# Kernel tuning notes

Measured on AMD Instinct MI355X. Metric: run time of the kernel, lower is better.

Reference implementation:

```python
import jax, jax.numpy as jnp
import numpy as np
from jax import lax

NUM_HEADS = 8  # init_kwargs: num_heads
TOPK = 7       # hard-coded in DMF.forward


def setup_inputs() -> dict:
    key = jax.random.key(0)
    k1, k2, k3, k4 = jax.random.split(key, 4)
    b, dim, H, W = 8, 384, 128, 128
    x = jax.random.normal(k1, (b, dim, H, W), dtype=jnp.float32)
    qkv_w = jax.random.normal(k2, (dim * 3, dim), dtype=jnp.float32) * 0.05   # 1x1 conv weight
    dw_w = jax.random.normal(k3, (dim * 3, 1, 3, 3), dtype=jnp.float32) * 0.05  # depthwise 3x3
    proj_w = jax.random.normal(k4, (dim, dim), dtype=jnp.float32) * 0.05     # 1x1 conv weight
    temperature = jnp.ones((NUM_HEADS, 1, 1), dtype=jnp.float32)
    return {"x": x, "qkv_w": qkv_w, "dw_w": dw_w, "proj_w": proj_w, "temperature": temperature}


def _l2norm(t, eps=1e-12):
    # matches torch.nn.functional.normalize(dim=-1)
    n = jnp.sqrt(jnp.sum(t * t, axis=-1, keepdims=True))
    return t / jnp.maximum(n, eps)


def reference(x, qkv_w, dw_w, proj_w, temperature):
    b, c, h, w = x.shape
    ch = c // NUM_HEADS  # channels per head

    # 1x1 conv (pointwise) -> depthwise 3x3 conv
    qkv = jnp.einsum('bchw,oc->bohw', x, qkv_w)
    qkv = lax.conv_general_dilated(
        qkv, dw_w, window_strides=(1, 1), padding=[(1, 1), (1, 1)],
        feature_group_count=qkv.shape[1],
        dimension_numbers=('NCHW', 'OIHW', 'NCHW'))
    q, k, v = jnp.split(qkv, 3, axis=1)

    def to_heads(t):  # b (head ch) h w -> b head ch (h w)
        return t.reshape(b, NUM_HEADS, ch, h * w)

    q = _l2norm(to_heads(q))
    k = _l2norm(to_heads(k))
    v = to_heads(v)

    # channel attention: [b, head, ch, ch]
    attn_weight = jnp.einsum('bhcn,bhdn->bhcd', q, k) * temperature

    # top-k sparsify along last dim, then masked softmax
    _, idx = lax.top_k(attn_weight, TOPK)                      # [b,h,ch,TOPK]
    cols = jnp.arange(attn_weight.shape[-1])
    mask = (idx[..., None] == cols).any(axis=-2)               # [b,h,ch,ch] bool
    attn = jnp.where(mask, attn_weight, -jnp.inf)
    attn = jax.nn.softmax(attn, axis=-1)

    out = jnp.einsum('bhcd,bhdn->bhcn', attn, v).reshape(b, c, h, w)
    out = jnp.einsum('bchw,oc->bohw', out, proj_w)
    return out
```

## Files before the change

kernel.cpp:

```cpp
#include <hip/hip_runtime.h>

#define HWN 16384
#define WDIM 128

typedef __bf16 bf16x8 __attribute__((ext_vector_type(8)));
typedef __bf16 bf16x4 __attribute__((ext_vector_type(4)));
typedef __bf16 bf16x2 __attribute__((ext_vector_type(2)));
typedef float floatx4 __attribute__((ext_vector_type(4)));

#define LSTR 36

__global__ __launch_bounds__(256, 2) void gemm_mfma3(
    const __bf16* __restrict__ Ah, const __bf16* __restrict__ Al,
    const float* __restrict__ B, float* __restrict__ C,
    int K, long sA, long sB, long sC) {
  __shared__ __bf16 sAh[128 * LSTR], sAl[128 * LSTR], sBh[128 * LSTR], sBl[128 * LSTR];
  const int bz = blockIdx.z;
  Ah += (long)bz * sA;
  Al += (long)bz * sA;
  B += (long)bz * sB;
  C += (long)bz * sC;
  const int tid = threadIdx.x;
  const int n0 = blockIdx.x << 7, m0 = blockIdx.y << 7;
  const int arow = tid >> 1, akq = (tid & 1) << 4;
  const int bn = (tid & 63) << 1;
  const int bkb = (tid >> 6) << 3;
  const int lane = tid & 63, wv = tid >> 6;
  const int mq = (wv & 1) << 6, nq = (wv >> 1) << 6;
  const int fm = lane & 15, fq = lane >> 4;
  floatx4 acc[4][4] = {};
  for (int k0 = 0; k0 < K; k0 += 32) {
    const __bf16* pAh = Ah + (long)(m0 + arow) * K + k0 + akq;
    const __bf16* pAl = Al + (long)(m0 + arow) * K + k0 + akq;
    bf16x8 a0 = *(const bf16x8*)pAh;
    bf16x8 a1 = *(const bf16x8*)(pAh + 8);
    bf16x8 a2 = *(const bf16x8*)pAl;
    bf16x8 a3 = *(const bf16x8*)(pAl + 8);
    const float* pB = B + (long)(k0 + bkb) * HWN + n0 + bn;
    float2 v[8];
#pragma unroll
    for (int r = 0; r < 8; ++r) v[r] = *(const float2*)(pB + (long)r * HWN);
    bf16x8 bh0, bh1, bl0, bl1;
#pragma unroll
    for (int r = 0; r < 8; ++r) {
      float vx = v[r].x, vy = v[r].y;
      __bf16 hx = (__bf16)vx, hy = (__bf16)vy;
      bh0[r] = hx;
      bh1[r] = hy;
      bl0[r] = (__bf16)(vx - (float)hx);
      bl1[r] = (__bf16)(vy - (float)hy);
    }
    __syncthreads();
    *(bf16x8*)&sAh[arow * LSTR + akq] = a0;
    *(bf16x8*)&sAh[arow * LSTR + akq + 8] = a1;
    *(bf16x8*)&sAl[arow * LSTR + akq] = a2;
    *(bf16x8*)&sAl[arow * LSTR + akq + 8] = a3;
    *(bf16x8*)&sBh[bn * LSTR + bkb] = bh0;
    *(bf16x8*)&sBh[(bn + 1) * LSTR + bkb] = bh1;
    *(bf16x8*)&sBl[bn * LSTR + bkb] = bl0;
    *(bf16x8*)&sBl[(bn + 1) * LSTR + bkb] = bl1;
    __syncthreads();
    bf16x8 fAh[4], fAl[4];
#pragma unroll
    for (int i = 0; i < 4; ++i) {
      fAh[i] = *(const bf16x8*)&sAh[(mq + i * 16 + fm) * LSTR + fq * 8];
      fAl[i] = *(const bf16x8*)&sAl[(mq + i * 16 + fm) * LSTR + fq * 8];
    }
#pragma unroll
    for (int j = 0; j < 4; ++j) {
      bf16x8 bh = *(const bf16x8*)&sBh[(nq + j * 16 + fm) * LSTR + fq * 8];
      bf16x8 bl = *(const bf16x8*)&sBl[(nq + j * 16 + fm) * LSTR + fq * 8];
#pragma unroll
      for (int i = 0; i < 4; ++i) {
        acc[i][j] = __builtin_amdgcn_mfma_f32_16x16x32_bf16(fAh[i], bh, acc[i][j], 0, 0, 0);
        acc[i][j] = __builtin_amdgcn_mfma_f32_16x16x32_bf16(fAl[i], bh, acc[i][j], 0, 0, 0);
        acc[i][j] = __builtin_amdgcn_mfma_f32_16x16x32_bf16(fAh[i], bl, acc[i][j], 0, 0, 0);
      }
    }
  }
#pragma unroll
  for (int i = 0; i < 4; ++i)
#pragma unroll
    for (int j = 0; j < 4; ++j) {
      const int col = n0 + nq + j * 16 + fm;
#pragma unroll
      for (int r = 0; r < 4; ++r) {
        const int row = m0 + mq + i * 16 + fq * 4 + r;
        C[(long)row * HWN + col] = acc[i][j][r];
      }
    }
}

__global__ __launch_bounds__(256, 2) void gemm_bf3(
    const __bf16* __restrict__ Ah, const __bf16* __restrict__ Al,
    const __bf16* __restrict__ Bh, const __bf16* __restrict__ Bl,
    float* __restrict__ C, int K, long sA, long sB, long sC) {
  __shared__ __bf16 sAh[128 * LSTR], sAl[128 * LSTR], sBh[128 * LSTR], sBl[128 * LSTR];
  const int bz = blockIdx.z;
  Ah += (long)bz * sA;
  Al += (long)bz * sA;
  Bh += (long)bz * sB;
  Bl += (long)bz * sB;
  C += (long)bz * sC;
  const int tid = threadIdx.x;
  const int n0 = blockIdx.x << 7, m0 = blockIdx.y << 7;
  const int arow = tid >> 1, akq = (tid & 1) << 4;
  const int bn = (tid & 63) << 1;
  const int bkb = (tid >> 6) << 3;
  const int lane = tid & 63, wv = tid >> 6;
  const int mq = (wv & 1) << 6, nq = (wv >> 1) << 6;
  const int fm = lane & 15, fq = lane >> 4;
  floatx4 acc[4][4] = {};
  for (int k0 = 0; k0 < K; k0 += 32) {
    const __bf16* pAh = Ah + (long)(m0 + arow) * K + k0 + akq;
    const __bf16* pAl = Al + (long)(m0 + arow) * K + k0 + akq;
    bf16x8 a0 = *(const bf16x8*)pAh;
    bf16x8 a1 = *(const bf16x8*)(pAh + 8);
    bf16x8 a2 = *(const bf16x8*)pAl;
    bf16x8 a3 = *(const bf16x8*)(pAl + 8);
    const __bf16* pBh = Bh + (long)(k0 + bkb) * HWN + n0 + bn;
    const __bf16* pBl = Bl + (long)(k0 + bkb) * HWN + n0 + bn;
    bf16x2 vh[8], vl[8];
#pragma unroll
    for (int r = 0; r < 8; ++r) {
      vh[r] = *(const bf16x2*)(pBh + (long)r * HWN);
      vl[r] = *(const bf16x2*)(pBl + (long)r * HWN);
    }
    bf16x8 bh0, bh1, bl0, bl1;
#pragma unroll
    for (int r = 0; r < 8; ++r) {
      bh0[r] = vh[r][0];
      bh1[r] = vh[r][1];
      bl0[r] = vl[r][0];
      bl1[r] = vl[r][1];
    }
    __syncthreads();
    *(bf16x8*)&sAh[arow * LSTR + akq] = a0;
    *(bf16x8*)&sAh[arow * LSTR + akq + 8] = a1;
    *(bf16x8*)&sAl[arow * LSTR + akq] = a2;
    *(bf16x8*)&sAl[arow * LSTR + akq + 8] = a3;
    *(bf16x8*)&sBh[bn * LSTR + bkb] = bh0;
    *(bf16x8*)&sBh[(bn + 1) * LSTR + bkb] = bh1;
    *(bf16x8*)&sBl[bn * LSTR + bkb] = bl0;
    *(bf16x8*)&sBl[(bn + 1) * LSTR + bkb] = bl1;
    __syncthreads();
    bf16x8 fAh[4], fAl[4];
#pragma unroll
    for (int i = 0; i < 4; ++i) {
      fAh[i] = *(const bf16x8*)&sAh[(mq + i * 16 + fm) * LSTR + fq * 8];
      fAl[i] = *(const bf16x8*)&sAl[(mq + i * 16 + fm) * LSTR + fq * 8];
    }
#pragma unroll
    for (int j = 0; j < 4; ++j) {
      bf16x8 bh = *(const bf16x8*)&sBh[(nq + j * 16 + fm) * LSTR + fq * 8];
      bf16x8 bl = *(const bf16x8*)&sBl[(nq + j * 16 + fm) * LSTR + fq * 8];
#pragma unroll
      for (int i = 0; i < 4; ++i) {
        acc[i][j] = __builtin_amdgcn_mfma_f32_16x16x32_bf16(fAh[i], bh, acc[i][j], 0, 0, 0);
        acc[i][j] = __builtin_amdgcn_mfma_f32_16x16x32_bf16(fAl[i], bh, acc[i][j], 0, 0, 0);
        acc[i][j] = __builtin_amdgcn_mfma_f32_16x16x32_bf16(fAh[i], bl, acc[i][j], 0, 0, 0);
      }
    }
  }
#pragma unroll
  for (int i = 0; i < 4; ++i)
#pragma unroll
    for (int j = 0; j < 4; ++j) {
      const int col = n0 + nq + j * 16 + fm;
#pragma unroll
      for (int r = 0; r < 4; ++r) {
        const int row = m0 + mq + i * 16 + fq * 4 + r;
        C[(long)row * HWN + col] = acc[i][j][r];
      }
    }
}

__global__ __launch_bounds__(256) void split_w(
    const float* __restrict__ w, __bf16* __restrict__ hi, __bf16* __restrict__ lo, int n) {
  int i = blockIdx.x * 256 + threadIdx.x;
  if (i < n) {
    float v = w[i];
    __bf16 h = (__bf16)v;
    hi[i] = h;
    lo[i] = (__bf16)(v - (float)h);
  }
}

__global__ __launch_bounds__(256) void dw_split(
    const float* __restrict__ qkv1, const float* __restrict__ dww,
    __bf16* __restrict__ dwh, __bf16* __restrict__ dwl,
    float* __restrict__ qs, float* __restrict__ ks, int b0) {
  const int tid = threadIdx.x;
  const int ch = blockIdx.x;
  const int yh = blockIdx.y;
  const int bz = blockIdx.z;
  const int xg = tid & 31;
  const int rg = tid >> 5;
  const float4* P = (const float4*)(qkv1 + ((long)bz * 1152 + ch) * HWN);
  const float* wp = dww + (long)ch * 9;
  const float w00 = wp[0], w01 = wp[1], w02 = wp[2];
  const float w10 = wp[3], w11 = wp[4], w12 = wp[5];
  const float w20 = wp[6], w21 = wp[7], w22 = wp[8];
  const int y0 = (yh << 6) + (rg << 3);
  float4 vr[10];
#pragma unroll
  for (int r = 0; r < 10; ++r) {
    int yy = y0 - 1 + r;
    vr[r] = make_float4(0.f, 0.f, 0.f, 0.f);
    if (yy >= 0 && yy < WDIM) vr[r] = P[yy * 32 + xg];
  }
  float lf[10], rt[10];
#pragma unroll
  for (int r = 0; r < 10; ++r) {
    float l_ = __shfl_up(vr[r].w, 1, 64);
    float r_ = __shfl_down(vr[r].x, 1, 64);
    lf[r] = (xg == 0) ? 0.f : l_;
    rt[r] = (xg == 31) ? 0.f : r_;
  }
  const long obase = ((long)bz * 1152 + ch) * HWN;
  float sq = 0.f;
#pragma unroll
  for (int i = 0; i < 8; ++i) {
    const float t0 = lf[i], t1 = vr[i].x, t2 = vr[i].y, t3 = vr[i].z, t4 = vr[i].w, t5 = rt[i];
    const float m0_ = lf[i + 1], m1 = vr[i + 1].x, m2 = vr[i + 1].y, m3 = vr[i + 1].z,
                m4 = vr[i + 1].w, m5 = rt[i + 1];
    const float b0_ = lf[i + 2], b1 = vr[i + 2].x, b2 = vr[i + 2].y, b3 = vr[i + 2].z,
                b4 = vr[i + 2].w, b5 = rt[i + 2];
    float o0 = w00 * t0 + w01 * t1 + w02 * t2 + w10 * m0_ + w11 * m1 + w12 * m2 +
               w20 * b0_ + w21 * b1 + w22 * b2;
    float o1 = w00 * t1 + w01 * t2 + w02 * t3 + w10 * m1 + w11 * m2 + w12 * m3 +
               w20 * b1 + w21 * b2 + w22 * b3;
    float o2 = w00 * t2 + w01 * t3 + w02 * t4 + w10 * m2 + w11 * m3 + w12 * m4 +
               w20 * b2 + w21 * b3 + w22 * b4;
    float o3 = w00 * t3 + w01 * t4 + w02 * t5 + w10 * m3 + w11 * m4 + w12 * m5 +
               w20 * b3 + w21 * b4 + w22 * b5;
    sq += o0 * o0 + o1 * o1 + o2 * o2 + o3 * o3;
    bf16x4 h4, l4;
    __bf16 h0 = (__bf16)o0, h1 = (__bf16)o1, h2 = (__bf16)o2, h3 = (__bf16)o3;
    h4[0] = h0; h4[1] = h1; h4[2] = h2; h4[3] = h3;
    l4[0] = (__bf16)(o0 - (float)h0);
    l4[1] = (__bf16)(o1 - (float)h1);
    l4[2] = (__bf16)(o2 - (float)h2);
    l4[3] = (__bf16)(o3 - (float)h3);
    long off = obase + (y0 + i) * WDIM + xg * 4;
    *(bf16x4*)&dwh[off] = h4;
    *(bf16x4*)&dwl[off] = l4;
  }
  if (ch < 768) {
#pragma unroll
    for (int off = 32; off >= 1; off >>= 1) sq += __shfl_down(sq, off, 64);
    if ((tid & 63) == 0) {
      int b = b0 + bz;
      if (ch < 384)
        atomicAdd(qs + b * 384 + ch, sq);
      else
        atomicAdd(ks + b * 384 + (ch - 384), sq);
    }
  }
}

__global__ __launch_bounds__(256) void gram_mfma(
    const __bf16* __restrict__ dwh, const __bf16* __restrict__ dwl,
    float* __restrict__ gram, int b0) {
  __shared__ float R[4][2304];
  const int tid = threadIdx.x, lane = tid & 63, wv = tid >> 6;
  const int pc = blockIdx.x, h = blockIdx.y, bz = blockIdx.z;
  const __bf16* Qh = dwh + ((long)bz * 1152 + h * 48) * HWN;
  const __bf16* Ql = dwl + ((long)bz * 1152 + h * 48) * HWN;
  const __bf16* Kh = dwh + ((long)bz * 1152 + 384 + h * 48) * HWN;
  const __bf16* Kl = dwl + ((long)bz * 1152 + 384 + h * 48) * HWN;
  const int fm = lane & 15;
  const int fk = (lane >> 4) << 3;
  floatx4 acc[3][3] = {};
  const int pend = pc * 1024 + wv * 256 + 256;
  for (int p0 = pc * 1024 + wv * 256; p0 < pend; p0 += 32) {
    bf16x8 ah[3], al[3], bh[3], bl[3];
#pragma unroll
    for (int i = 0; i < 3; ++i) {
      const long ro = (long)(i * 16 + fm) * HWN + p0 + fk;
      ah[i] = *(const bf16x8*)(Qh + ro);
      al[i] = *(const bf16x8*)(Ql + ro);
      bh[i] = *(const bf16x8*)(Kh + ro);
      bl[i] = *(const bf16x8*)(Kl + ro);
    }
#pragma unroll
    for (int i = 0; i < 3; ++i)
#pragma unroll
      for (int j = 0; j < 3; ++j) {
        acc[i][j] = __builtin_amdgcn_mfma_f32_16x16x32_bf16(ah[i], bh[j], acc[i][j], 0, 0, 0);
        acc[i][j] = __builtin_amdgcn_mfma_f32_16x16x32_bf16(al[i], bh[j], acc[i][j], 0, 0, 0);
        acc[i][j] = __builtin_amdgcn_mfma_f32_16x16x32_bf16(ah[i], bl[j], acc[i][j], 0, 0, 0);
      }
  }
#pragma unroll
  for (int i = 0; i < 3; ++i)
#pragma unroll
    for (int j = 0; j < 3; ++j)
#pragma unroll
      for (int r = 0; r < 4; ++r)
        R[wv][(i * 16 + (lane >> 4) * 4 + r) * 48 + j * 16 + fm] = acc[i][j][r];
  __syncthreads();
  float* gb = gram + (long)((b0 + bz) * 8 + h) * 2304;
  for (int idx = tid; idx < 2304; idx += 256) {
    float s = R[0][idx] + R[1][idx] + R[2][idx] + R[3][idx];
    atomicAdd(gb + idx, s);
  }
}

__global__ __launch_bounds__(256) void attn_M(
    const float* __restrict__ gram, const float* __restrict__ qs, const float* __restrict__ ks,
    const float* __restrict__ temp, const float* __restrict__ pw,
    __bf16* __restrict__ Mh, __bf16* __restrict__ Ml, int b0) {
  const int z = blockIdx.x;
  const int b = b0 + (z >> 3), h = z & 7;
  __shared__ float kn[48];
  __shared__ float at[48][49];
  const int tid = threadIdx.x;
  if (tid < 48) kn[tid] = fmaxf(sqrtf(ks[b * 384 + h * 48 + tid]), 1e-12f);
  __syncthreads();
  if (tid < 48) {
    const int c = tid;
    float qn = fmaxf(sqrtf(qs[b * 384 + h * 48 + c]), 1e-12f);
    float tv = temp[h];
    const float* gr = gram + (long)(b * 8 + h) * 2304 + c * 48;
    float s[48];
#pragma unroll
    for (int d = 0; d < 48; ++d) s[d] = gr[d] / (qn * kn[d]) * tv;
    unsigned long long sel = 0ull;
    float m0 = 0.f;
    for (int it = 0; it < 7; ++it) {
      float mx = -3.0e38f;
      int mi = 0;
#pragma unroll
      for (int d = 0; d < 48; ++d) {
        bool taken = (sel >> d) & 1ull;
        if (!taken && s[d] > mx) { mx = s[d]; mi = d; }
      }
      sel |= (1ull << mi);
      if (it == 0) m0 = mx;
    }
    float sum = 0.f;
    float e[48];
#pragma unroll
    for (int d = 0; d < 48; ++d) {
      bool t = (sel >> d) & 1ull;
      float ev = t ? expf(s[d] - m0) : 0.f;
      e[d] = ev;
      sum += ev;
    }
    float inv = 1.f / sum;
#pragma unroll
    for (int d = 0; d < 48; ++d) at[c][d] = e[d] * inv;
  }
  __syncthreads();
  for (int idx = tid; idx < 384 * 48; idx += 256) {
    int o = idx / 48, d = idx % 48;
    const float* pr = pw + (long)o * 384 + h * 48;
    float acc = 0.f;
#pragma unroll
    for (int c = 0; c < 48; ++c) acc += pr[c] * at[c][d];
    long oi = ((long)b * 384 + o) * 384 + h * 48 + d;
    __bf16 hh = (__bf16)acc;
    Mh[oi] = hh;
    Ml[oi] = (__bf16)(acc - (float)hh);
  }
}

extern "C" void kernel_launch(void* const* d_in, const int* in_sizes, int n_in,
                              void* d_out, int out_size, void* d_ws, size_t ws_size,
                              hipStream_t stream) {
  const float* x = (const float*)d_in[0];
  const float* qkv_w = (const float*)d_in[1];
  const float* dw_w = (const float*)d_in[2];
  const float* proj_w = (const float*)d_in[3];
  const float* temp = (const float*)d_in[4];
  float* out = (float*)d_out;
  float* ws = (float*)d_ws;

  float* gram = ws;
  float* qs = gram + 147456;
  float* ks = qs + 3072;
  __bf16* Wh = (__bf16*)(ks + 3072);
  __bf16* Wl = Wh + 442368;
  __bf16* Mh = Wl + 442368;
  __bf16* Ml = Mh + 1179648;
  float* qkv1 = (float*)(Ml + 1179648);
  const long SMALLS = 1775616L;
  const long PERB = 37748736L;
  long wsf = (long)(ws_size / 4);
  int nb = (int)((wsf - SMALLS) / PERB);
  if (nb < 1) nb = 1;
  if (nb > 8) nb = 8;
  __bf16* dwh = (__bf16*)(qkv1 + (long)nb * 18874368L);
  __bf16* dwl = dwh + (long)nb * 18874368L;

  hipMemsetAsync(gram, 0, (147456 + 3072 + 3072) * sizeof(float), stream);
  split_w<<<dim3((442368 + 255) / 256), 256, 0, stream>>>(qkv_w, Wh, Wl, 442368);

  for (int b0 = 0; b0 < 8; b0 += nb) {
    int nbc = (8 - b0 < nb) ? (8 - b0) : nb;
    gemm_mfma3<<<dim3(128, 9, nbc), 256, 0, stream>>>(
        Wh, Wl, x + (long)b0 * 6291456L, qkv1, 384, 0L, 6291456L, 18874368L);
    dw_split<<<dim3(1152, 2, nbc), 256, 0, stream>>>(qkv1, dw_w, dwh, dwl, qs, ks, b0);
    gram_mfma<<<dim3(16, 8, nbc), 256, 0, stream>>>(dwh, dwl, gram, b0);
    attn_M<<<dim3(nbc * 8), 256, 0, stream>>>(gram, qs, ks, temp, proj_w, Mh, Ml, b0);
    gemm_bf3<<<dim3(128, 3, nbc), 256, 0, stream>>>(
        Mh + (long)b0 * 147456L, Ml + (long)b0 * 147456L,
        dwh + 768L * HWN, dwl + 768L * HWN,
        out + (long)b0 * 6291456L, 384, 147456L, 18874368L, 6291456L);
  }
}
```

Baseline: 1.325 ms.

## Pre-split x into bf16 hi/lo and double gram kernel parallelism

Removes the fused fp32-load-and-split QKV GEMM. A separate split_x pass now converts x into bf16 hi/lo buffers, and the QKV projection reuses the generic bf16 three-pass GEMM. This drops the per-block conversion of B tiles, which each of the 9 M-tiles repeated, at the cost of an extra pass over x and more workspace per batch, which may reduce the batch chunk size. Separately, the gram kernel gets twice as many blocks, each covering half the pixels, to raise occupancy at the cost of more atomic reductions.

```diff
diff --git a/kernel.cpp b/kernel.cpp
--- a/kernel.cpp
+++ b/kernel.cpp
@@ -9,87 +9,6 @@
 typedef float floatx4 __attribute__((ext_vector_type(4)));
 
 #define LSTR 36
-
-__global__ __launch_bounds__(256, 2) void gemm_mfma3(
-    const __bf16* __restrict__ Ah, const __bf16* __restrict__ Al,
-    const float* __restrict__ B, float* __restrict__ C,
-    int K, long sA, long sB, long sC) {
-  __shared__ __bf16 sAh[128 * LSTR], sAl[128 * LSTR], sBh[128 * LSTR], sBl[128 * LSTR];
-  const int bz = blockIdx.z;
-  Ah += (long)bz * sA;
-  Al += (long)bz * sA;
-  B += (long)bz * sB;
-  C += (long)bz * sC;
-  const int tid = threadIdx.x;
-  const int n0 = blockIdx.x << 7, m0 = blockIdx.y << 7;
-  const int arow = tid >> 1, akq = (tid & 1) << 4;
-  const int bn = (tid & 63) << 1;
-  const int bkb = (tid >> 6) << 3;
-  const int lane = tid & 63, wv = tid >> 6;
-  const int mq = (wv & 1) << 6, nq = (wv >> 1) << 6;
-  const int fm = lane & 15, fq = lane >> 4;
-  floatx4 acc[4][4] = {};
-  for (int k0 = 0; k0 < K; k0 += 32) {
-    const __bf16* pAh = Ah + (long)(m0 + arow) * K + k0 + akq;
-    const __bf16* pAl = Al + (long)(m0 + arow) * K + k0 + akq;
-    bf16x8 a0 = *(const bf16x8*)pAh;
-    bf16x8 a1 = *(const bf16x8*)(pAh + 8);
-    bf16x8 a2 = *(const bf16x8*)pAl;
-    bf16x8 a3 = *(const bf16x8*)(pAl + 8);
-    const float* pB = B + (long)(k0 + bkb) * HWN + n0 + bn;
-    float2 v[8];
-#pragma unroll
-    for (int r = 0; r < 8; ++r) v[r] = *(const float2*)(pB + (long)r * HWN);
-    bf16x8 bh0, bh1, bl0, bl1;
-#pragma unroll
-    for (int r = 0; r < 8; ++r) {
-      float vx = v[r].x, vy = v[r].y;
-      __bf16 hx = (__bf16)vx, hy = (__bf16)vy;
-      bh0[r] = hx;
-      bh1[r] = hy;
-      bl0[r] = (__bf16)(vx - (float)hx);
-      bl1[r] = (__bf16)(vy - (float)hy);
-    }
-    __syncthreads();
-    *(bf16x8*)&sAh[arow * LSTR + akq] = a0;
-    *(bf16x8*)&sAh[arow * LSTR + akq + 8] = a1;
-    *(bf16x8*)&sAl[arow * LSTR + akq] = a2;
-    *(bf16x8*)&sAl[arow * LSTR + akq + 8] = a3;
-    *(bf16x8*)&sBh[bn * LSTR + bkb] = bh0;
-    *(bf16x8*)&sBh[(bn + 1) * LSTR + bkb] = bh1;
-    *(bf16x8*)&sBl[bn * LSTR + bkb] = bl0;
-    *(bf16x8*)&sBl[(bn + 1) * LSTR + bkb] = bl1;
-    __syncthreads();
-    bf16x8 fAh[4], fAl[4];
-#pragma unroll
-    for (int i = 0; i < 4; ++i) {
-      fAh[i] = *(const bf16x8*)&sAh[(mq + i * 16 + fm) * LSTR + fq * 8];
-      fAl[i] = *(const bf16x8*)&sAl[(mq + i * 16 + fm) * LSTR + fq * 8];
-    }
-#pragma unroll
-    for (int j = 0; j < 4; ++j) {
-      bf16x8 bh = *(const bf16x8*)&sBh[(nq + j * 16 + fm) * LSTR + fq * 8];
-      bf16x8 bl = *(const bf16x8*)&sBl[(nq + j * 16 + fm) * LSTR + fq * 8];
-#pragma unroll
-      for (int i = 0; i < 4; ++i) {
-        acc[i][j] = __builtin_amdgcn_mfma_f32_16x16x32_bf16(fAh[i], bh, acc[i][j], 0, 0, 0);
-        acc[i][j] = __builtin_amdgcn_mfma_f32_16x16x32_bf16(fAl[i], bh, acc[i][j], 0, 0, 0);
-        acc[i][j] = __builtin_amdgcn_mfma_f32_16x16x32_bf16(fAh[i], bl, acc[i][j], 0, 0, 0);
-      }
-    }
-  }
-#pragma unroll
-  for (int i = 0; i < 4; ++i)
-#pragma unroll
-    for (int j = 0; j < 4; ++j) {
-      const int col = n0 + nq + j * 16 + fm;
-#pragma unroll
-      for (int r = 0; r < 4; ++r) {
-        const int row = m0 + mq + i * 16 + fq * 4 + r;
-        C[(long)row * HWN + col] = acc[i][j][r];
-      }
-    }
-}
 
 __global__ __launch_bounds__(256, 2) void gemm_bf3(
     const __bf16* __restrict__ Ah, const __bf16* __restrict__ Al,
@@ -186,6 +105,23 @@
   }
 }
 
+__global__ __launch_bounds__(256) void split_x(
+    const float* __restrict__ w, __bf16* __restrict__ hi, __bf16* __restrict__ lo, long n4) {
+  long i = (long)blockIdx.x * 256 + threadIdx.x;
+  if (i < n4) {
+    float4 v = *(const float4*)(w + i * 4);
+    bf16x4 h4, l4;
+    __bf16 h0 = (__bf16)v.x, h1 = (__bf16)v.y, h2 = (__bf16)v.z, h3 = (__bf16)v.w;
+    h4[0] = h0; h4[1] = h1; h4[2] = h2; h4[3] = h3;
+    l4[0] = (__bf16)(v.x - (float)h0);
+    l4[1] = (__bf16)(v.y - (float)h1);
+    l4[2] = (__bf16)(v.z - (float)h2);
+    l4[3] = (__bf16)(v.w - (float)h3);
+    *(bf16x4*)&hi[i * 4] = h4;
+    *(bf16x4*)&lo[i * 4] = l4;
+  }
+}
+
 __global__ __launch_bounds__(256) void dw_split(
     const float* __restrict__ qkv1, const float* __restrict__ dww,
     __bf16* __restrict__ dwh, __bf16* __restrict__ dwl,
@@ -272,8 +208,8 @@
   const int fm = lane & 15;
   const int fk = (lane >> 4) << 3;
   floatx4 acc[3][3] = {};
-  const int pend = pc * 1024 + wv * 256 + 256;
-  for (int p0 = pc * 1024 + wv * 256; p0 < pend; p0 += 32) {
+  const int pstart = pc * 512 + wv * 128;
+  for (int p0 = pstart; p0 < pstart + 128; p0 += 32) {
     bf16x8 ah[3], al[3], bh[3], bl[3];
 #pragma unroll
     for (int i = 0; i < 3; ++i) {
@@ -386,23 +322,27 @@
   __bf16* Ml = Mh + 1179648;
   float* qkv1 = (float*)(Ml + 1179648);
   const long SMALLS = 1775616L;
-  const long PERB = 37748736L;
+  const long PERB = 44040192L;
   long wsf = (long)(ws_size / 4);
   int nb = (int)((wsf - SMALLS) / PERB);
   if (nb < 1) nb = 1;
   if (nb > 8) nb = 8;
   __bf16* dwh = (__bf16*)(qkv1 + (long)nb * 18874368L);
   __bf16* dwl = dwh + (long)nb * 18874368L;
+  __bf16* Xh = dwl + (long)nb * 18874368L;
+  __bf16* Xl = Xh + (long)nb * 6291456L;
 
   hipMemsetAsync(gram, 0, (147456 + 3072 + 3072) * sizeof(float), stream);
   split_w<<<dim3((442368 + 255) / 256), 256, 0, stream>>>(qkv_w, Wh, Wl, 442368);
 
   for (int b0 = 0; b0 < 8; b0 += nb) {
     int nbc = (8 - b0 < nb) ? (8 - b0) : nb;
-    gemm_mfma3<<<dim3(128, 9, nbc), 256, 0, stream>>>(
-        Wh, Wl, x + (long)b0 * 6291456L, qkv1, 384, 0L, 6291456L, 18874368L);
+    split_x<<<dim3(nbc * 6144), 256, 0, stream>>>(
+        x + (long)b0 * 6291456L, Xh, Xl, (long)nbc * 1572864L);
+    gemm_bf3<<<dim3(128, 9, nbc), 256, 0, stream>>>(
+        Wh, Wl, Xh, Xl, qkv1, 384, 0L, 6291456L, 18874368L);
     dw_split<<<dim3(1152, 2, nbc), 256, 0, stream>>>(qkv1, dw_w, dwh, dwl, qs, ks, b0);
-    gram_mfma<<<dim3(16, 8, nbc), 256, 0, stream>>>(dwh, dwl, gram, b0);
+    gram_mfma<<<dim3(32, 8, nbc), 256, 0, stream>>>(dwh, dwl, gram, b0);
     attn_M<<<dim3(nbc * 8), 256, 0, stream>>>(gram, qs, ks, temp, proj_w, Mh, Ml, b0);
     gemm_bf3<<<dim3(128, 3, nbc), 256, 0, stream>>>(
         Mh + (long)b0 * 147456L, Ml + (long)b0 * 147456L,
```

New measurement: 1.390 ms. 4.9% more time.

## Retile depthwise conv per full channel and double gram grid with MFMA priority

Applied to the files above, without the earlier changes.

The depthwise conv kernel now has one block cover a whole channel image, with each thread computing 16 rows instead of 8. Halo shuffles are done as a rolling window to cut redundant halo loads and shuffles. The gram kernel splits the pixel range into twice as many blocks, each with a fully unrolled 4-step loop, and raises wave priority around the MFMA bursts. This trades lower dw_split parallelism and higher register use for less halo overhead, and gives gram more blocks at the cost of more atomic reductions.

```diff
diff --git a/kernel.cpp b/kernel.cpp
--- a/kernel.cpp
+++ b/kernel.cpp
@@ -192,8 +192,7 @@
     float* __restrict__ qs, float* __restrict__ ks, int b0) {
   const int tid = threadIdx.x;
   const int ch = blockIdx.x;
-  const int yh = blockIdx.y;
-  const int bz = blockIdx.z;
+  const int bz = blockIdx.y;
   const int xg = tid & 31;
   const int rg = tid >> 5;
   const float4* P = (const float4*)(qkv1 + ((long)bz * 1152 + ch) * HWN);
@@ -201,31 +200,35 @@
   const float w00 = wp[0], w01 = wp[1], w02 = wp[2];
   const float w10 = wp[3], w11 = wp[4], w12 = wp[5];
   const float w20 = wp[6], w21 = wp[7], w22 = wp[8];
-  const int y0 = (yh << 6) + (rg << 3);
-  float4 vr[10];
-#pragma unroll
-  for (int r = 0; r < 10; ++r) {
+  const int y0 = rg << 4;
+  float4 vr[18];
+#pragma unroll
+  for (int r = 0; r < 18; ++r) {
     int yy = y0 - 1 + r;
     vr[r] = make_float4(0.f, 0.f, 0.f, 0.f);
     if (yy >= 0 && yy < WDIM) vr[r] = P[yy * 32 + xg];
   }
-  float lf[10], rt[10];
-#pragma unroll
-  for (int r = 0; r < 10; ++r) {
-    float l_ = __shfl_up(vr[r].w, 1, 64);
-    float r_ = __shfl_down(vr[r].x, 1, 64);
-    lf[r] = (xg == 0) ? 0.f : l_;
-    rt[r] = (xg == 31) ? 0.f : r_;
-  }
+  float lA = __shfl_up(vr[0].w, 1, 64);
+  float rA = __shfl_down(vr[0].x, 1, 64);
+  if (xg == 0) lA = 0.f;
+  if (xg == 31) rA = 0.f;
+  float lB = __shfl_up(vr[1].w, 1, 64);
+  float rB = __shfl_down(vr[1].x, 1, 64);
+  if (xg == 0) lB = 0.f;
+  if (xg == 31) rB = 0.f;
   const long obase = ((long)bz * 1152 + ch) * HWN;
   float sq = 0.f;
 #pragma unroll
-  for (int i = 0; i < 8; ++i) {
-    const float t0 = lf[i], t1 = vr[i].x, t2 = vr[i].y, t3 = vr[i].z, t4 = vr[i].w, t5 = rt[i];
-    const float m0_ = lf[i + 1], m1 = vr[i + 1].x, m2 = vr[i + 1].y, m3 = vr[i + 1].z,
-                m4 = vr[i + 1].w, m5 = rt[i + 1];
-    const float b0_ = lf[i + 2], b1 = vr[i + 2].x, b2 = vr[i + 2].y, b3 = vr[i + 2].z,
-                b4 = vr[i + 2].w, b5 = rt[i + 2];
+  for (int i = 0; i < 16; ++i) {
+    float lC = __shfl_up(vr[i + 2].w, 1, 64);
+    float rC = __shfl_down(vr[i + 2].x, 1, 64);
+    if (xg == 0) lC = 0.f;
+    if (xg == 31) rC = 0.f;
+    const float t0 = lA, t1 = vr[i].x, t2 = vr[i].y, t3 = vr[i].z, t4 = vr[i].w, t5 = rA;
+    const float m0_ = lB, m1 = vr[i + 1].x, m2 = vr[i + 1].y, m3 = vr[i + 1].z,
+                m4 = vr[i + 1].w, m5 = rB;
+    const float b0_ = lC, b1 = vr[i + 2].x, b2 = vr[i + 2].y, b3 = vr[i + 2].z,
+                b4 = vr[i + 2].w, b5 = rC;
     float o0 = w00 * t0 + w01 * t1 + w02 * t2 + w10 * m0_ + w11 * m1 + w12 * m2 +
                w20 * b0_ + w21 * b1 + w22 * b2;
     float o1 = w00 * t1 + w01 * t2 + w02 * t3 + w10 * m1 + w11 * m2 + w12 * m3 +
@@ -245,6 +248,8 @@
     long off = obase + (y0 + i) * WDIM + xg * 4;
     *(bf16x4*)&dwh[off] = h4;
     *(bf16x4*)&dwl[off] = l4;
+    lA = lB; rA = rB;
+    lB = lC; rB = rC;
   }
   if (ch < 768) {
 #pragma unroll
@@ -272,8 +277,10 @@
   const int fm = lane & 15;
   const int fk = (lane >> 4) << 3;
   floatx4 acc[3][3] = {};
-  const int pend = pc * 1024 + wv * 256 + 256;
-  for (int p0 = pc * 1024 + wv * 256; p0 < pend; p0 += 32) {
+  const int pstart = pc * 512 + wv * 128;
+#pragma unroll
+  for (int s = 0; s < 4; ++s) {
+    const int p0 = pstart + s * 32;
     bf16x8 ah[3], al[3], bh[3], bl[3];
 #pragma unroll
     for (int i = 0; i < 3; ++i) {
@@ -283,6 +290,7 @@
       bh[i] = *(const bf16x8*)(Kh + ro);
       bl[i] = *(const bf16x8*)(Kl + ro);
     }
+    __builtin_amdgcn_s_setprio(1);
 #pragma unroll
     for (int i = 0; i < 3; ++i)
 #pragma unroll
@@ -291,6 +299,7 @@
         acc[i][j] = __builtin_amdgcn_mfma_f32_16x16x32_bf16(al[i], bh[j], acc[i][j], 0, 0, 0);
         acc[i][j] = __builtin_amdgcn_mfma_f32_16x16x32_bf16(ah[i], bl[j], acc[i][j], 0, 0, 0);
       }
+    __builtin_amdgcn_s_setprio(0);
   }
 #pragma unroll
   for (int i = 0; i < 3; ++i)
@@ -401,8 +410,8 @@
     int nbc = (8 - b0 < nb) ? (8 - b0) : nb;
     gemm_mfma3<<<dim3(128, 9, nbc), 256, 0, stream>>>(
         Wh, Wl, x + (long)b0 * 6291456L, qkv1, 384, 0L, 6291456L, 18874368L);
-    dw_split<<<dim3(1152, 2, nbc), 256, 0, stream>>>(qkv1, dw_w, dwh, dwl, qs, ks, b0);
-    gram_mfma<<<dim3(16, 8, nbc), 256, 0, stream>>>(dwh, dwl, gram, b0);
+    dw_split<<<dim3(1152, nbc), 256, 0, stream>>>(qkv1, dw_w, dwh, dwl, qs, ks, b0);
+    gram_mfma<<<dim3(32, 8, nbc), 256, 0, stream>>>(dwh, dwl, gram, b0);
     attn_M<<<dim3(nbc * 8), 256, 0, stream>>>(gram, qs, ks, temp, proj_w, Mh, Ml, b0);
     gemm_bf3<<<dim3(128, 3, nbc), 256, 0, stream>>>(
         Mh + (long)b0 * 147456L, Ml + (long)b0 * 147456L,
```

After: 1.321 ms. No clear change (-0.4%).
